# Performance work log

Hardware: AMD Instinct MI355X
Metric: run time of the kernel (lower is better)

The kernel has to match this reference:

```python
import jax, jax.numpy as jnp
import numpy as np

B, S, H, QKV, NH, MLP = 4, 2048, 512, 512, 8, 2048
HD = QKV // NH
EPS = 1e-6


def _layernorm(x):
    # LayerNorm over last dim, no affine, eps=1e-6
    mu = jnp.mean(x, axis=-1, keepdims=True)
    var = jnp.mean(jnp.square(x - mu), axis=-1, keepdims=True)
    return (x - mu) * jax.lax.rsqrt(var + EPS)


def setup_inputs() -> dict:
    key = jax.random.key(0)
    ks = jax.random.split(key, 8)
    sc_in = 1.0 / np.sqrt(H)
    sc_qkv = 1.0 / np.sqrt(QKV)
    sc_mlp = 1.0 / np.sqrt(MLP)
    return {
        "input": jax.random.normal(ks[0], (B, S, H), dtype=jnp.float32),
        "mask": jnp.ones((B, S), dtype=jnp.float32),
        "Wq": jax.random.normal(ks[1], (H, QKV), dtype=jnp.float32) * sc_in,
        "Wk": jax.random.normal(ks[2], (H, QKV), dtype=jnp.float32) * sc_in,
        "Wv": jax.random.normal(ks[3], (H, QKV), dtype=jnp.float32) * sc_in,
        "Wo": jax.random.normal(ks[4], (QKV, H), dtype=jnp.float32) * sc_qkv,
        "W1": jax.random.normal(ks[5], (H, MLP), dtype=jnp.float32) * sc_in,
        "W2": jax.random.normal(ks[6], (MLP, H), dtype=jnp.float32) * sc_mlp,
    }


def reference(input, mask, Wq, Wk, Wv, Wo, W1, W2):
    # pre-mask + pre-norm
    x = input * mask[..., None]
    x = _layernorm(x)
    # qkv projections, split heads: [B,S,QKV] -> [B,NH,S,HD]
    def heads(t):
        return t.reshape(B, S, NH, HD).transpose(0, 2, 1, 3)
    q = heads(x @ Wq) * (1.0 / np.sqrt(HD))
    k = heads(x @ Wk)
    v = heads(x @ Wv)
    logits = jnp.einsum("bhqd,bhkd->bhqk", q, k)  # [B,NH,S,S]
    amask = mask[:, None, :, None]  # 'b q -> b 1 q 1'
    logits = logits + (-100000.0) * (1.0 - amask)
    att = jax.nn.softmax(logits, axis=-1)
    out = jnp.einsum("bhqk,bhkd->bhqd", att, v)
    out = out.transpose(0, 2, 1, 3).reshape(B, S, QKV)
    x = input + out @ Wo  # residual
    x = x * mask[..., None]
    y = _layernorm(x)
    ffn = jax.nn.gelu(y @ W1, approximate=False) @ W2
    return ffn + x
```

## Files before the change

kernel.cpp:

```cpp
#include <hip/hip_runtime.h>
#include <hip/hip_bf16.h>
#include <cmath>

typedef __attribute__((ext_vector_type(8))) short bf16x8;
typedef __attribute__((ext_vector_type(4))) float f32x4;
typedef __attribute__((ext_vector_type(16))) float f32x16;
typedef unsigned short u16;
typedef unsigned int u32;

#define B_ 4
#define S_ 2048
#define H_ 512
#define NH_ 8
#define HD_ 64
#define MLP_ 2048
#define M_ (B_*S_)

__device__ __forceinline__ float bf2f(u16 u){ u32 v=((u32)u)<<16; float f; __builtin_memcpy(&f,&v,4); return f; }
__device__ __forceinline__ u16 f2bf(float f){ u32 u; __builtin_memcpy(&u,&f,4); u32 r=(u+0x7fffu+((u>>16)&1u))>>16; return (u16)r; }
__device__ __forceinline__ u32 pk2(float lo, float hi2){
  __hip_bfloat162 t = __float22bfloat162_rn(make_float2(lo, hi2));
  u32 r; __builtin_memcpy(&r, &t, 4); return r;
}

__device__ __forceinline__ float xhalf_add(float x){
  float a = x, b = x;
  asm volatile("v_permlane32_swap_b32 %0, %1" : "+v"(a), "+v"(b));
  return a + b;
}

__device__ __forceinline__ void gl16(const u16* g, u16* l) {
  __builtin_amdgcn_global_load_lds((const __attribute__((address_space(1))) u32*)(g),
                                   (__attribute__((address_space(3))) u32*)(l), 16, 0, 0);
}

__device__ __forceinline__ void gemm_core(
    const u16* __restrict__ A, const u16* __restrict__ Bt,
    int lda, int ldb, int nkt, int m0, int n0,
    u16* As, u16* Bs, f32x4 (&acc)[4][4])
{
  const int tid = threadIdx.x;
  const int lane = tid & 63;
  const int w = tid >> 6;
  const int lr = lane & 15;
  const int g  = lane >> 4;
  const int wr = w >> 1, wc = w & 1;

  const int sr = lane >> 3;
  const int scol = ((lane & 7) ^ sr) << 3;

  int aoff[2][4], boff[2][4];
#pragma unroll
  for (int m = 0; m < 4; ++m) {
    int ra = wr*64 + m*16 + lr;
    int rb = wc*64 + m*16 + lr;
#pragma unroll
    for (int kk = 0; kk < 2; ++kk) {
      aoff[kk][m] = ra*64 + (((kk*4+g) ^ (ra&7))<<3);
      boff[kk][m] = rb*64 + (((kk*4+g) ^ (rb&7))<<3);
    }
  }
  const u16* Ap = A + (size_t)m0*lda;
  const u16* Bp = Bt + (size_t)n0*ldb;

#pragma unroll
  for (int c = 0; c < 4; ++c) {
    gl16(Ap + (size_t)(w*32 + c*8 + sr)*lda + scol, As + w*2048 + c*512);
    gl16(Bp + (size_t)(w*32 + c*8 + sr)*ldb + scol, Bs + w*2048 + c*512);
  }

  for (int kt = 0; kt < nkt; ++kt) {
    const int cb = (kt & 1) * 8192;
    if (kt + 1 < nkt) {
      const int k0 = (kt + 1) << 6;
      const int nb = ((kt + 1) & 1) * 8192;
#pragma unroll
      for (int c = 0; c < 4; ++c) {
        gl16(Ap + (size_t)(w*32 + c*8 + sr)*lda + k0 + scol, As + nb + w*2048 + c*512);
        gl16(Bp + (size_t)(w*32 + c*8 + sr)*ldb + k0 + scol, Bs + nb + w*2048 + c*512);
      }
      asm volatile("s_waitcnt vmcnt(8)" ::: "memory");
    } else {
      asm volatile("s_waitcnt vmcnt(0)" ::: "memory");
    }
    __builtin_amdgcn_s_barrier();

#pragma unroll
    for (int kk = 0; kk < 2; ++kk) {
      bf16x8 af[4], bfr[4];
#pragma unroll
      for (int m = 0; m < 4; ++m) {
        af[m]  = *(const bf16x8*)(As + cb + aoff[kk][m]);
        bfr[m] = *(const bf16x8*)(Bs + cb + boff[kk][m]);
      }
#pragma unroll
      for (int m = 0; m < 4; ++m) {
#pragma unroll
        for (int n = 0; n < 4; ++n) {
          acc[m][n] = __builtin_amdgcn_mfma_f32_16x16x32_bf16(af[m], bfr[n], acc[m][n], 0, 0, 0);
        }
      }
    }
    __builtin_amdgcn_s_barrier();
  }
}

__device__ __forceinline__ void gemm_core64(
    const u16* __restrict__ A, const u16* __restrict__ Bt,
    int lda, int ldb, int nkt, int m0, int n0,
    u16* As, u16* Bs, f32x4 (&acc)[2][4])
{
  const int tid = threadIdx.x;
  const int lane = tid & 63;
  const int w = tid >> 6;
  const int lr = lane & 15;
  const int g  = lane >> 4;

  const int sr = lane >> 3;
  const int scol = ((lane & 7) ^ sr) << 3;

  int aoff[2][2], boff[2][4];
#pragma unroll
  for (int m = 0; m < 2; ++m) {
    int ra = w*32 + m*16 + lr;
#pragma unroll
    for (int kk = 0; kk < 2; ++kk) aoff[kk][m] = ra*64 + (((kk*4+g) ^ (ra&7))<<3);
  }
#pragma unroll
  for (int n = 0; n < 4; ++n) {
    int rb = n*16 + lr;
#pragma unroll
    for (int kk = 0; kk < 2; ++kk) boff[kk][n] = rb*64 + (((kk*4+g) ^ (rb&7))<<3);
  }
  const u16* Ap = A + (size_t)m0*lda;
  const u16* Bp = Bt + (size_t)n0*ldb;

#pragma unroll
  for (int c = 0; c < 4; ++c)
    gl16(Ap + (size_t)(w*32 + c*8 + sr)*lda + scol, As + w*2048 + c*512);
#pragma unroll
  for (int c = 0; c < 2; ++c)
    gl16(Bp + (size_t)(w*16 + c*8 + sr)*ldb + scol, Bs + w*1024 + c*512);

  for (int kt = 0; kt < nkt; ++kt) {
    const int cbA = (kt & 1) * 8192;
    const int cbB = (kt & 1) * 4096;
    if (kt + 1 < nkt) {
      const int k0 = (kt + 1) << 6;
      const int nbA = ((kt + 1) & 1) * 8192;
      const int nbB = ((kt + 1) & 1) * 4096;
#pragma unroll
      for (int c = 0; c < 4; ++c)
        gl16(Ap + (size_t)(w*32 + c*8 + sr)*lda + k0 + scol, As + nbA + w*2048 + c*512);
#pragma unroll
      for (int c = 0; c < 2; ++c)
        gl16(Bp + (size_t)(w*16 + c*8 + sr)*ldb + k0 + scol, Bs + nbB + w*1024 + c*512);
      asm volatile("s_waitcnt vmcnt(6)" ::: "memory");
    } else {
      asm volatile("s_waitcnt vmcnt(0)" ::: "memory");
    }
    __builtin_amdgcn_s_barrier();

#pragma unroll
    for (int kk = 0; kk < 2; ++kk) {
      bf16x8 af[2], bfr[4];
#pragma unroll
      for (int m = 0; m < 2; ++m) af[m] = *(const bf16x8*)(As + cbA + aoff[kk][m]);
#pragma unroll
      for (int n = 0; n < 4; ++n) bfr[n] = *(const bf16x8*)(Bs + cbB + boff[kk][n]);
#pragma unroll
      for (int m = 0; m < 2; ++m) {
#pragma unroll
        for (int n = 0; n < 4; ++n) {
          acc[m][n] = __builtin_amdgcn_mfma_f32_16x16x32_bf16(af[m], bfr[n], acc[m][n], 0, 0, 0);
        }
      }
    }
    __builtin_amdgcn_s_barrier();
  }
}

__global__ __launch_bounds__(256,2) void k_qkv(
    const u16* __restrict__ xn, const u16* __restrict__ wqt,
    const u16* __restrict__ wkt, const u16* __restrict__ wvt,
    u16* __restrict__ q, u16* __restrict__ k, u16* __restrict__ v)
{
  __shared__ u16 As[2*128*64], Bs[2*128*64];
  int m0 = blockIdx.x*128;
  int sel = blockIdx.y >> 2;
  int n0 = (blockIdx.y & 3)*128;
  const u16* Bt = sel==0 ? wqt : (sel==1 ? wkt : wvt);
  u16* O = sel==0 ? q : (sel==1 ? k : v);
  float alpha = (sel==0) ? 0.125f : 1.0f;
  f32x4 acc[4][4] = {};
  gemm_core(xn, Bt, H_, H_, H_/64, m0, n0, As, Bs, acc);
  const int lane = threadIdx.x&63, w = threadIdx.x>>6;
  const int lr = lane&15, g = lane>>4, wr = w>>1, wc = w&1;
#pragma unroll
  for (int m=0;m<4;++m) {
#pragma unroll
    for (int n=0;n<4;++n) {
#pragma unroll
      for (int r=0;r<4;++r) {
        int row = m0 + wr*64 + m*16 + g*4 + r;
        int col = n0 + wc*64 + n*16 + lr;
        O[(size_t)row*H_ + col] = f2bf(acc[m][n][r]*alpha);
      }
    }
  }
}

template<int EPI>
__global__ __launch_bounds__(256,2) void k_gemm(
    const u16* __restrict__ A, const u16* __restrict__ Bt, void* __restrict__ Ov,
    const float* __restrict__ aux, const float* __restrict__ maskv,
    int N, int K)
{
  __shared__ u16 As[2*128*64], Bs[2*128*64];
  int m0 = blockIdx.x*128, n0 = blockIdx.y*128;
  f32x4 acc[4][4] = {};
  gemm_core(A, Bt, K, K, K>>6, m0, n0, As, Bs, acc);
  const int lane = threadIdx.x&63, w = threadIdx.x>>6;
  const int lr = lane&15, g = lane>>4, wr = w>>1, wc = w&1;
#pragma unroll
  for (int m=0;m<4;++m) {
#pragma unroll
    for (int n=0;n<4;++n) {
#pragma unroll
      for (int r=0;r<4;++r) {
        int row = m0 + wr*64 + m*16 + g*4 + r;
        int col = n0 + wc*64 + n*16 + lr;
        float val = acc[m][n][r];
        if (EPI == 1) {
          val = 0.5f*val*(1.0f + erff(val*0.70710678118654752f));
          ((u16*)Ov)[(size_t)row*N + col] = f2bf(val);
        } else if (EPI == 2) {
          float mv = maskv[row];
          val = (aux[(size_t)row*N + col] + val)*mv;
          ((float*)Ov)[(size_t)row*N + col] = val;
        } else if (EPI == 3) {
          val += aux[(size_t)row*N + col];
          ((float*)Ov)[(size_t)row*N + col] = val;
        }
      }
    }
  }
}

template<int EPI>
__global__ __launch_bounds__(256,3) void k_gemm64(
    const u16* __restrict__ A, const u16* __restrict__ Bt, void* __restrict__ Ov,
    const float* __restrict__ aux, const float* __restrict__ maskv,
    int N, int K)
{
  __shared__ u16 As[2*128*64], Bs[2*64*64];
  int m0 = blockIdx.x*128, n0 = blockIdx.y*64;
  f32x4 acc[2][4] = {};
  gemm_core64(A, Bt, K, K, K>>6, m0, n0, As, Bs, acc);
  const int lane = threadIdx.x&63, w = threadIdx.x>>6;
  const int lr = lane&15, g = lane>>4;
#pragma unroll
  for (int m=0;m<2;++m) {
#pragma unroll
    for (int n=0;n<4;++n) {
#pragma unroll
      for (int r=0;r<4;++r) {
        int row = m0 + w*32 + m*16 + g*4 + r;
        int col = n0 + n*16 + lr;
        float val = acc[m][n][r];
        if (EPI == 2) {
          float mv = maskv[row];
          val = (aux[(size_t)row*N + col] + val)*mv;
          ((float*)Ov)[(size_t)row*N + col] = val;
        } else if (EPI == 3) {
          val += aux[(size_t)row*N + col];
          ((float*)Ov)[(size_t)row*N + col] = val;
        }
      }
    }
  }
}

template<int MASKED>
__global__ __launch_bounds__(256) void k_ln(const float* __restrict__ in,
    const float* __restrict__ mask, u16* __restrict__ out)
{
  int row = blockIdx.x*4 + (threadIdx.x>>6);
  int lane = threadIdx.x & 63;
  const f32x4* p = (const f32x4*)(in + (size_t)row*H_ + lane*8);
  f32x4 a = p[0], b = p[1];
  float mv = MASKED ? mask[row] : 1.0f;
  float x[8]; float s = 0.f, s2 = 0.f;
#pragma unroll
  for (int j=0;j<4;++j){ x[j] = a[j]*mv; x[4+j] = b[j]*mv; }
#pragma unroll
  for (int j=0;j<8;++j){ s += x[j]; s2 += x[j]*x[j]; }
#pragma unroll
  for (int m=1;m<32;m<<=1){ s += __shfl_xor(s,m); s2 += __shfl_xor(s2,m); }
  s = xhalf_add(s); s2 = xhalf_add(s2);
  float mu = s*(1.0f/H_);
  float var = s2*(1.0f/H_) - mu*mu;
  float inv = rsqrtf(var + 1e-6f);
  bf16x8 o;
#pragma unroll
  for (int j=0;j<8;++j) o[j] = (short)f2bf((x[j]-mu)*inv);
  *(bf16x8*)(out + (size_t)row*H_ + lane*8) = o;
}

__global__ void k_tr4(const float* __restrict__ s0, const float* __restrict__ s1,
                      const float* __restrict__ s2, const float* __restrict__ s3,
                      u16* __restrict__ d0, u16* __restrict__ d1,
                      u16* __restrict__ d2, u16* __restrict__ d3)
{
  __shared__ u16 t[32][33];
  const float* src = blockIdx.z==0 ? s0 : (blockIdx.z==1 ? s1 : (blockIdx.z==2 ? s2 : s3));
  u16* dst = blockIdx.z==0 ? d0 : (blockIdx.z==1 ? d1 : (blockIdx.z==2 ? d2 : d3));
  int c0 = blockIdx.x*32, r0 = blockIdx.y*32;
  int tx = threadIdx.x & 31, ty = threadIdx.x >> 5;
#pragma unroll
  for (int i=0;i<32;i+=8) t[ty+i][tx] = f2bf(src[(size_t)(r0+ty+i)*512 + c0+tx]);
  __syncthreads();
#pragma unroll
  for (int i=0;i<32;i+=8) dst[(size_t)(c0+ty+i)*512 + r0+tx] = t[tx][ty+i];
}

__global__ void k_tr(const float* __restrict__ src, u16* __restrict__ dst, int R, int C)
{
  __shared__ u16 t[32][33];
  int c0 = blockIdx.x*32, r0 = blockIdx.y*32;
  int tx = threadIdx.x & 31, ty = threadIdx.x >> 5;
#pragma unroll
  for (int i=0;i<32;i+=8) t[ty+i][tx] = f2bf(src[(size_t)(r0+ty+i)*C + c0+tx]);
  __syncthreads();
#pragma unroll
  for (int i=0;i<32;i+=8) dst[(size_t)(c0+ty+i)*R + r0+tx] = t[tx][ty+i];
}

__global__ void k_trv(const u16* __restrict__ v, u16* __restrict__ vt)
{
  __shared__ u16 t[32][33];
  int bh = blockIdx.z, b = bh>>3, h = bh&7;
  int s0 = blockIdx.x*32, d0 = blockIdx.y*32;
  int tx = threadIdx.x & 31, ty = threadIdx.x >> 5;
#pragma unroll
  for (int i=0;i<32;i+=8) t[ty+i][tx] = v[(size_t)(b*S_ + s0+ty+i)*H_ + h*HD_ + d0+tx];
  __syncthreads();
#pragma unroll
  for (int i=0;i<32;i+=8) vt[((size_t)bh*HD_ + d0+ty+i)*S_ + s0+tx] = t[tx][ty+i];
}

__global__ __launch_bounds__(256) void k_attn(
    const u16* __restrict__ q, const u16* __restrict__ kmat,
    const u16* __restrict__ vt, const float* __restrict__ mask,
    u16* __restrict__ o)
{
  __shared__ u16 Ks[2][64*64];
  __shared__ u16 Vs[2][64*64];
  __shared__ float bias[S_];
  __shared__ float lsums[4][32];

  const int tid = threadIdx.x;
  const int lane = tid & 63;
  const int w = tid >> 6;
  const int l31 = lane & 31;
  const int hi = lane >> 5;
  const int bh = blockIdx.y, b = bh >> 3, h = bh & 7;
  const int q0 = blockIdx.x * 128;

  const int sr = lane >> 3;
  const int sl = (lane & 7) ^ (sr & 7);
  const u16* ks0 = kmat + (size_t)(b*S_ + w*16 + sr)*H_ + h*HD_ + sl*8;
  const u16* ks1 = ks0 + (size_t)8*H_;
  const u16* vs0 = vt + ((size_t)bh*HD_ + w*16 + sr)*S_ + sl*8;
  const u16* vs1 = vs0 + (size_t)8*S_;

  {
    u16* kd = &Ks[0][0] + w*1024;
    u16* vd = &Vs[0][0] + w*1024;
    gl16(ks0, kd); gl16(ks1, kd + 512);
    gl16(vs0, vd); gl16(vs1, vd + 512);
  }

  for (int j = tid; j < S_; j += 256) bias[j] = -100000.0f * (1.0f - mask[b*S_ + j]);

  bf16x8 qf[4];
  {
    const u16* qp = q + (size_t)(b*S_ + q0 + w*32 + l31)*H_ + h*HD_ + hi*8;
#pragma unroll
    for (int ds = 0; ds < 4; ++ds) qf[ds] = *(const bf16x8*)(qp + ds*16);
  }

  f32x16 po0 = {}, po1 = {};
  float mreg = -1e30f, lsum = 0.f;

  __syncthreads();

  for (int jt = 0; jt < 32; ++jt) {
    const int buf = jt & 1;
    if (jt < 31) {
      const int j0 = (jt + 1) * 64;
      u16* kd = &Ks[buf ^ 1][0] + w*1024;
      u16* vd = &Vs[buf ^ 1][0] + w*1024;
      gl16(ks0 + (size_t)j0*H_, kd); gl16(ks1 + (size_t)j0*H_, kd + 512);
      gl16(vs0 + j0, vd);            gl16(vs1 + j0, vd + 512);
      asm volatile("s_waitcnt vmcnt(4)" ::: "memory");
    } else {
      asm volatile("s_waitcnt vmcnt(0)" ::: "memory");
    }
    __builtin_amdgcn_s_barrier();

    const u16* kt  = &Ks[buf][0];
    const u16* vtl = &Vs[buf][0];

    f32x16 s0, s1;
    const float* bp = &bias[jt*64 + hi*4];
#pragma unroll
    for (int kb = 0; kb < 2; ++kb) {
      f32x16 acc;
#pragma unroll
      for (int g2 = 0; g2 < 4; ++g2) {
        f32x4 b4 = *(const f32x4*)(bp + kb*32 + g2*8);
        acc[g2*4+0] = b4[0]; acc[g2*4+1] = b4[1];
        acc[g2*4+2] = b4[2]; acc[g2*4+3] = b4[3];
      }
      const int key = kb*32 + l31;
      const u16* kr = kt + key*64;
      __builtin_amdgcn_s_setprio(1);
#pragma unroll
      for (int ds = 0; ds < 4; ++ds) {
        bf16x8 kf = *(const bf16x8*)(kr + (((ds*2 + hi) ^ (key & 7)) << 3));
        acc = __builtin_amdgcn_mfma_f32_32x32x16_bf16(kf, qf[ds], acc, 0, 0, 0);
      }
      __builtin_amdgcn_s_setprio(0);
      if (kb == 0) s0 = acc; else s1 = acc;
    }

    float mx = s0[0];
#pragma unroll
    for (int r = 1; r < 16; ++r) mx = fmaxf(mx, s0[r]);
#pragma unroll
    for (int r = 0; r < 16; ++r) mx = fmaxf(mx, s1[r]);
    mx = fmaxf(mx, __shfl_xor(mx, 32));
    if (__any(mx > mreg + 8.0f)) {
      float mn = fmaxf(mreg, mx);
      float sc = __expf(mreg - mn);
      lsum *= sc;
#pragma unroll
      for (int r = 0; r < 16; ++r) { po0[r] *= sc; po1[r] *= sc; }
      mreg = mn;
    }
    float ps = 0.f;
#pragma unroll
    for (int r = 0; r < 16; ++r) { float p = __expf(s0[r]-mreg); s0[r] = p; ps += p; }
#pragma unroll
    for (int r = 0; r < 16; ++r) { float p = __expf(s1[r]-mreg); s1[r] = p; ps += p; }
    ps += __shfl_xor(ps, 32);
    lsum += ps;

#pragma unroll
    for (int kb = 0; kb < 2; ++kb) {
      const f32x16& sv = kb ? s1 : s0;
      u32 w01 = pk2(sv[0],  sv[1]);
      u32 w23 = pk2(sv[2],  sv[3]);
      u32 w45 = pk2(sv[4],  sv[5]);
      u32 w67 = pk2(sv[6],  sv[7]);
      asm volatile("v_permlane32_swap_b32 %0, %1" : "+v"(w01), "+v"(w45));
      asm volatile("v_permlane32_swap_b32 %0, %1" : "+v"(w23), "+v"(w67));
      u32 w89 = pk2(sv[8],  sv[9]);
      u32 wab = pk2(sv[10], sv[11]);
      u32 wcd = pk2(sv[12], sv[13]);
      u32 wef = pk2(sv[14], sv[15]);
      asm volatile("v_permlane32_swap_b32 %0, %1" : "+v"(w89), "+v"(wcd));
      asm volatile("v_permlane32_swap_b32 %0, %1" : "+v"(wab), "+v"(wef));
      union { u32 wrd[4]; bf16x8 v; } f0, f1;
      f0.wrd[0]=w01; f0.wrd[1]=w23; f0.wrd[2]=w45; f0.wrd[3]=w67;
      f1.wrd[0]=w89; f1.wrd[1]=wab; f1.wrd[2]=wcd; f1.wrd[3]=wef;
      __builtin_amdgcn_s_setprio(1);
#pragma unroll
      for (int ks = 0; ks < 2; ++ks) {
        bf16x8 pa = ks ? f1.v : f0.v;
#pragma unroll
        for (int nb = 0; nb < 2; ++nb) {
          int dd = nb*32 + l31;
          int slot = ((kb*4 + ks*2 + hi) ^ (dd & 7)) << 3;
          bf16x8 vf = *(const bf16x8*)(vtl + dd*64 + slot);
          if (nb == 0) po0 = __builtin_amdgcn_mfma_f32_32x32x16_bf16(pa, vf, po0, 0,0,0);
          else         po1 = __builtin_amdgcn_mfma_f32_32x32x16_bf16(pa, vf, po1, 0,0,0);
        }
      }
      __builtin_amdgcn_s_setprio(0);
    }
    __builtin_amdgcn_s_barrier();
  }

  if (hi == 0) lsums[w][l31] = lsum;
  f32x4 li[4];
#pragma unroll
  for (int g2i = 0; g2i < 4; ++g2i) {
    f32x4 t = *(const f32x4*)&lsums[w][g2i*8 + hi*4];
    li[g2i][0] = 1.0f/t[0]; li[g2i][1] = 1.0f/t[1];
    li[g2i][2] = 1.0f/t[2]; li[g2i][3] = 1.0f/t[3];
  }
  u16* op = o + (size_t)(b*S_ + q0 + w*32)*H_ + h*HD_;
#pragma unroll
  for (int nb = 0; nb < 2; ++nb) {
#pragma unroll
    for (int r = 0; r < 16; ++r) {
      int row = (r&3) + 8*(r>>2) + 4*hi;
      float val = (nb ? po1[r] : po0[r]) * li[r>>2][r&3];
      op[(size_t)row*H_ + nb*32 + l31] = f2bf(val);
    }
  }
}

extern "C" void kernel_launch(void* const* d_in, const int* in_sizes, int n_in,
                              void* d_out, int out_size, void* d_ws, size_t ws_size,
                              hipStream_t stream) {
  const float* input = (const float*)d_in[0];
  const float* mask  = (const float*)d_in[1];
  const float* Wq = (const float*)d_in[2];
  const float* Wk = (const float*)d_in[3];
  const float* Wv = (const float*)d_in[4];
  const float* Wo = (const float*)d_in[5];
  const float* W1 = (const float*)d_in[6];
  const float* W2 = (const float*)d_in[7];
  float* out = (float*)d_out;
  u16* ws = (u16*)d_ws;

  u16* wqt = ws;
  u16* wkt = wqt + 262144;
  u16* wvt = wkt + 262144;
  u16* wot = wvt + 262144;
  u16* w1t = wot + 262144;
  u16* w2t = w1t + 1048576;
  u16* xn  = w2t + 1048576;
  u16* q   = xn  + 4194304;
  u16* k   = q   + 4194304;
  u16* v   = k   + 4194304;
  u16* vt  = v   + 4194304;
  u16*   attn = xn;
  float* x2f  = (float*)q;
  u16*   y    = v;
  u16*   h1   = vt;

  dim3 blk(256);
  k_tr4<<<dim3(16,16,4), blk, 0, stream>>>(Wq, Wk, Wv, Wo, wqt, wkt, wvt, wot);
  k_tr<<<dim3(64,16), blk, 0, stream>>>(W1, w1t, 512, 2048);
  k_tr<<<dim3(16,64), blk, 0, stream>>>(W2, w2t, 2048, 512);

  k_ln<1><<<2048, blk, 0, stream>>>(input, mask, xn);
  k_qkv<<<dim3(64,12), blk, 0, stream>>>(xn, wqt, wkt, wvt, q, k, v);
  k_trv<<<dim3(64,2,32), blk, 0, stream>>>(v, vt);
  k_attn<<<dim3(16,32), blk, 0, stream>>>(q, k, vt, mask, attn);
  k_gemm64<2><<<dim3(64,8), blk, 0, stream>>>(attn, wot, (void*)x2f, input, mask, 512, 512);
  k_ln<0><<<2048, blk, 0, stream>>>(x2f, nullptr, y);
  k_gemm<1><<<dim3(64,16), blk, 0, stream>>>(y, w1t, (void*)h1, nullptr, nullptr, 2048, 512);
  k_gemm64<3><<<dim3(64,8), blk, 0, stream>>>(h1, w2t, (void*)out, x2f, nullptr, 512, 2048);
}
```

Baseline: 192.7 us.

## Split attention keys into two halves with a combine pass, precompute mask bias

Attention now splits the key range into two halves over a new grid dimension, doubling block count from 512 to 1024 to fill more CUs. Each half writes unnormalized bf16 partial outputs plus per-row max and sum, and a new combine kernel merges them with log-sum-exp weights. The mask bias is precomputed once per batch into global memory with a flag, so bias loads are skipped when the mask has no zeros. This adds extra global traffic for the partials, an extra bf16 rounding, and two more kernel launches.

New measurement: 200.8 us. 1.04x slower.

```diff
diff --git a/kernel.cpp b/kernel.cpp
--- a/kernel.cpp
+++ b/kernel.cpp
@@ -349,15 +349,33 @@
   for (int i=0;i<32;i+=8) vt[((size_t)bh*HD_ + d0+ty+i)*S_ + s0+tx] = t[tx][ty+i];
 }
 
+__global__ void k_prep(const float* __restrict__ mask, float* __restrict__ biasf,
+                       u32* __restrict__ hb)
+{
+  __shared__ u32 f;
+  int b = blockIdx.x;
+  if (threadIdx.x == 0) f = 0;
+  __syncthreads();
+  bool any = false;
+  for (int j = threadIdx.x; j < S_; j += 256) {
+    float bv = -100000.0f * (1.0f - mask[b*S_ + j]);
+    biasf[b*S_ + j] = bv;
+    any |= (bv != 0.0f);
+  }
+  if (__ballot(any) != 0ull && (threadIdx.x & 63) == 0) atomicOr(&f, 1u);
+  __syncthreads();
+  if (threadIdx.x == 0) hb[b] = f;
+}
+
 __global__ __launch_bounds__(256) void k_attn(
     const u16* __restrict__ q, const u16* __restrict__ kmat,
-    const u16* __restrict__ vt, const float* __restrict__ mask,
-    u16* __restrict__ o)
+    const u16* __restrict__ vt, const float* __restrict__ biasf,
+    const u32* __restrict__ hb,
+    u16* __restrict__ pO0, u16* __restrict__ pO1,
+    float2* __restrict__ ml0, float2* __restrict__ ml1)
 {
   __shared__ u16 Ks[2][64*64];
   __shared__ u16 Vs[2][64*64];
-  __shared__ float bias[S_];
-  __shared__ float lsums[4][32];
 
   const int tid = threadIdx.x;
   const int lane = tid & 63;
@@ -366,12 +384,14 @@
   const int hi = lane >> 5;
   const int bh = blockIdx.y, b = bh >> 3, h = bh & 7;
   const int q0 = blockIdx.x * 128;
+  const int half = blockIdx.z;
+  const int k0g = half * 1024;
 
   const int sr = lane >> 3;
   const int sl = (lane & 7) ^ (sr & 7);
-  const u16* ks0 = kmat + (size_t)(b*S_ + w*16 + sr)*H_ + h*HD_ + sl*8;
+  const u16* ks0 = kmat + (size_t)(b*S_ + k0g + w*16 + sr)*H_ + h*HD_ + sl*8;
   const u16* ks1 = ks0 + (size_t)8*H_;
-  const u16* vs0 = vt + ((size_t)bh*HD_ + w*16 + sr)*S_ + sl*8;
+  const u16* vs0 = vt + ((size_t)bh*HD_ + w*16 + sr)*S_ + k0g + sl*8;
   const u16* vs1 = vs0 + (size_t)8*S_;
 
   {
@@ -381,7 +401,7 @@
     gl16(vs0, vd); gl16(vs1, vd + 512);
   }
 
-  for (int j = tid; j < S_; j += 256) bias[j] = -100000.0f * (1.0f - mask[b*S_ + j]);
+  const u32 hasb = hb[b];
 
   bf16x8 qf[4];
   {
@@ -395,9 +415,9 @@
 
   __syncthreads();
 
-  for (int jt = 0; jt < 32; ++jt) {
+  for (int jt = 0; jt < 16; ++jt) {
     const int buf = jt & 1;
-    if (jt < 31) {
+    if (jt < 15) {
       const int j0 = (jt + 1) * 64;
       u16* kd = &Ks[buf ^ 1][0] + w*1024;
       u16* vd = &Vs[buf ^ 1][0] + w*1024;
@@ -413,15 +433,17 @@
     const u16* vtl = &Vs[buf][0];
 
     f32x16 s0, s1;
-    const float* bp = &bias[jt*64 + hi*4];
 #pragma unroll
     for (int kb = 0; kb < 2; ++kb) {
-      f32x16 acc;
-#pragma unroll
-      for (int g2 = 0; g2 < 4; ++g2) {
-        f32x4 b4 = *(const f32x4*)(bp + kb*32 + g2*8);
-        acc[g2*4+0] = b4[0]; acc[g2*4+1] = b4[1];
-        acc[g2*4+2] = b4[2]; acc[g2*4+3] = b4[3];
+      f32x16 acc = {};
+      if (hasb) {
+        const float* bp = biasf + b*S_ + k0g + jt*64 + kb*32 + hi*4;
+#pragma unroll
+        for (int g2 = 0; g2 < 4; ++g2) {
+          f32x4 b4 = *(const f32x4*)(bp + g2*8);
+          acc[g2*4+0] = b4[0]; acc[g2*4+1] = b4[1];
+          acc[g2*4+2] = b4[2]; acc[g2*4+3] = b4[3];
+        }
       }
       const int key = kb*32 + l31;
       const u16* kr = kt + key*64;
@@ -493,24 +515,41 @@
     __builtin_amdgcn_s_barrier();
   }
 
-  if (hi == 0) lsums[w][l31] = lsum;
-  f32x4 li[4];
-#pragma unroll
-  for (int g2i = 0; g2i < 4; ++g2i) {
-    f32x4 t = *(const f32x4*)&lsums[w][g2i*8 + hi*4];
-    li[g2i][0] = 1.0f/t[0]; li[g2i][1] = 1.0f/t[1];
-    li[g2i][2] = 1.0f/t[2]; li[g2i][3] = 1.0f/t[3];
-  }
-  u16* op = o + (size_t)(b*S_ + q0 + w*32)*H_ + h*HD_;
+  u16* pOp = half ? pO1 : pO0;
+  float2* mlp = half ? ml1 : ml0;
+  u16* op = pOp + ((size_t)bh*S_ + q0 + w*32)*HD_;
 #pragma unroll
   for (int nb = 0; nb < 2; ++nb) {
 #pragma unroll
     for (int r = 0; r < 16; ++r) {
       int row = (r&3) + 8*(r>>2) + 4*hi;
-      float val = (nb ? po1[r] : po0[r]) * li[r>>2][r&3];
-      op[(size_t)row*H_ + nb*32 + l31] = f2bf(val);
-    }
-  }
+      op[(size_t)row*HD_ + nb*32 + l31] = f2bf(nb ? po1[r] : po0[r]);
+    }
+  }
+  if (hi == 0) mlp[(size_t)bh*S_ + q0 + w*32 + l31] = make_float2(mreg, lsum);
+}
+
+__global__ __launch_bounds__(256) void k_combine(
+    const u16* __restrict__ pO0, const u16* __restrict__ pO1,
+    const float2* __restrict__ ml0, const float2* __restrict__ ml1,
+    u16* __restrict__ o)
+{
+  const int bh = blockIdx.y, b = bh >> 3, h = bh & 7;
+  const int s = blockIdx.x*32 + (threadIdx.x >> 3);
+  const int dg = (threadIdx.x & 7) * 8;
+  float2 a = ml0[(size_t)bh*S_ + s];
+  float2 c = ml1[(size_t)bh*S_ + s];
+  float M = fmaxf(a.x, c.x);
+  float w0 = __expf(a.x - M), w1 = __expf(c.x - M);
+  float inv = 1.0f / (a.y*w0 + c.y*w1);
+  w0 *= inv; w1 *= inv;
+  bf16x8 f0 = *(const bf16x8*)(pO0 + ((size_t)bh*S_ + s)*HD_ + dg);
+  bf16x8 f1 = *(const bf16x8*)(pO1 + ((size_t)bh*S_ + s)*HD_ + dg);
+  bf16x8 r;
+#pragma unroll
+  for (int j = 0; j < 8; ++j)
+    r[j] = (short)f2bf(bf2f((u16)f0[j])*w0 + bf2f((u16)f1[j])*w1);
+  *(bf16x8*)(o + ((size_t)(b*S_ + s))*H_ + h*HD_ + dg) = r;
 }
 
 extern "C" void kernel_launch(void* const* d_in, const int* in_sizes, int n_in,
@@ -538,6 +577,12 @@
   u16* k   = q   + 4194304;
   u16* v   = k   + 4194304;
   u16* vt  = v   + 4194304;
+  u16*    pO0  = v;
+  u16*    pO1  = vt + 4194304;
+  float2* ml0  = (float2*)(pO1 + 4194304);
+  float2* ml1  = ml0 + 65536;
+  float*  biasf = (float*)(ml1 + 65536);
+  u32*    hbp   = (u32*)(biasf + B_*S_);
   u16*   attn = xn;
   float* x2f  = (float*)q;
   u16*   y    = v;
@@ -547,11 +592,13 @@
   k_tr4<<<dim3(16,16,4), blk, 0, stream>>>(Wq, Wk, Wv, Wo, wqt, wkt, wvt, wot);
   k_tr<<<dim3(64,16), blk, 0, stream>>>(W1, w1t, 512, 2048);
   k_tr<<<dim3(16,64), blk, 0, stream>>>(W2, w2t, 2048, 512);
+  k_prep<<<dim3(B_), blk, 0, stream>>>(mask, biasf, hbp);
 
   k_ln<1><<<2048, blk, 0, stream>>>(input, mask, xn);
   k_qkv<<<dim3(64,12), blk, 0, stream>>>(xn, wqt, wkt, wvt, q, k, v);
   k_trv<<<dim3(64,2,32), blk, 0, stream>>>(v, vt);
-  k_attn<<<dim3(16,32), blk, 0, stream>>>(q, k, vt, mask, attn);
+  k_attn<<<dim3(16,32,2), blk, 0, stream>>>(q, k, vt, biasf, hbp, pO0, pO1, ml0, ml1);
+  k_combine<<<dim3(64,32), blk, 0, stream>>>(pO0, pO1, ml0, ml1, attn);
   k_gemm64<2><<<dim3(64,8), blk, 0, stream>>>(attn, wot, (void*)x2f, input, mask, 512, 512);
   k_ln<0><<<2048, blk, 0, stream>>>(x2f, nullptr, y);
   k_gemm<1><<<dim3(64,16), blk, 0, stream>>>(y, w1t, (void*)h1, nullptr, nullptr, 2048, 512);
```

## Fuse V transpose into QKV epilogue, use exp2 softmax, merge weight transposes

Applied to the files above, without the earlier changes.

The QKV GEMM epilogue now writes V directly in transposed per-head layout, which removes the separate k_trv kernel and its extra read and write of V. Q is pre-scaled by log2(e) and the mask bias is scaled to match, so the attention softmax can use the native exp2 instruction instead of __expf. The two MLP weight-transpose launches are merged into a single launch. In exchange, the transposed V stores are 8-byte writes strided by S, which may coalesce poorly.

After: 184.2 us. -4.4%, faster.

```diff
diff --git a/kernel.cpp b/kernel.cpp
--- a/kernel.cpp
+++ b/kernel.cpp
@@ -3,6 +3,7 @@
 #include <cmath>
 
 typedef __attribute__((ext_vector_type(8))) short bf16x8;
+typedef __attribute__((ext_vector_type(4))) short u16x4;
 typedef __attribute__((ext_vector_type(4))) float f32x4;
 typedef __attribute__((ext_vector_type(16))) float f32x16;
 typedef unsigned short u16;
@@ -15,6 +16,7 @@
 #define HD_ 64
 #define MLP_ 2048
 #define M_ (B_*S_)
+#define LOG2E 1.44269504088896340736f
 
 __device__ __forceinline__ float bf2f(u16 u){ u32 v=((u32)u)<<16; float f; __builtin_memcpy(&f,&v,4); return f; }
 __device__ __forceinline__ u16 f2bf(float f){ u32 u; __builtin_memcpy(&u,&f,4); u32 r=(u+0x7fffu+((u>>16)&1u))>>16; return (u16)r; }
@@ -183,28 +185,45 @@
 __global__ __launch_bounds__(256,2) void k_qkv(
     const u16* __restrict__ xn, const u16* __restrict__ wqt,
     const u16* __restrict__ wkt, const u16* __restrict__ wvt,
-    u16* __restrict__ q, u16* __restrict__ k, u16* __restrict__ v)
+    u16* __restrict__ q, u16* __restrict__ k, u16* __restrict__ vt)
 {
   __shared__ u16 As[2*128*64], Bs[2*128*64];
   int m0 = blockIdx.x*128;
   int sel = blockIdx.y >> 2;
   int n0 = (blockIdx.y & 3)*128;
   const u16* Bt = sel==0 ? wqt : (sel==1 ? wkt : wvt);
-  u16* O = sel==0 ? q : (sel==1 ? k : v);
-  float alpha = (sel==0) ? 0.125f : 1.0f;
+  float alpha = (sel==0) ? 0.125f*LOG2E : 1.0f;
   f32x4 acc[4][4] = {};
   gemm_core(xn, Bt, H_, H_, H_/64, m0, n0, As, Bs, acc);
   const int lane = threadIdx.x&63, w = threadIdx.x>>6;
   const int lr = lane&15, g = lane>>4, wr = w>>1, wc = w&1;
-#pragma unroll
-  for (int m=0;m<4;++m) {
-#pragma unroll
-    for (int n=0;n<4;++n) {
-#pragma unroll
-      for (int r=0;r<4;++r) {
-        int row = m0 + wr*64 + m*16 + g*4 + r;
-        int col = n0 + wc*64 + n*16 + lr;
-        O[(size_t)row*H_ + col] = f2bf(acc[m][n][r]*alpha);
+  if (sel == 2) {
+#pragma unroll
+    for (int m=0;m<4;++m) {
+#pragma unroll
+      for (int n=0;n<4;++n) {
+        int rowb = m0 + wr*64 + m*16 + g*4;
+        int col  = n0 + wc*64 + n*16 + lr;
+        int b = rowb >> 11, s = rowb & 2047;
+        int h = col >> 6, d = col & 63;
+        u16x4 t;
+#pragma unroll
+        for (int r=0;r<4;++r) t[r] = (short)f2bf(acc[m][n][r]);
+        *(u16x4*)(vt + ((size_t)((b*NH_ + h)*HD_ + d))*S_ + s) = t;
+      }
+    }
+  } else {
+    u16* O = sel==0 ? q : k;
+#pragma unroll
+    for (int m=0;m<4;++m) {
+#pragma unroll
+      for (int n=0;n<4;++n) {
+#pragma unroll
+        for (int r=0;r<4;++r) {
+          int row = m0 + wr*64 + m*16 + g*4 + r;
+          int col = n0 + wc*64 + n*16 + lr;
+          O[(size_t)row*H_ + col] = f2bf(acc[m][n][r]*alpha);
+        }
       }
     }
   }
@@ -324,29 +343,23 @@
   for (int i=0;i<32;i+=8) dst[(size_t)(c0+ty+i)*512 + r0+tx] = t[tx][ty+i];
 }
 
-__global__ void k_tr(const float* __restrict__ src, u16* __restrict__ dst, int R, int C)
+__global__ void k_tr2(const float* __restrict__ W1, const float* __restrict__ W2,
+                      u16* __restrict__ d1, u16* __restrict__ d2)
 {
   __shared__ u16 t[32][33];
-  int c0 = blockIdx.x*32, r0 = blockIdx.y*32;
+  int z = blockIdx.z;
+  const float* src = z ? W2 : W1;
+  u16* dst = z ? d2 : d1;
+  int R = z ? 2048 : 512;
+  int C = z ? 512 : 2048;
+  int c0 = (z ? blockIdx.y : blockIdx.x) * 32;
+  int r0 = (z ? blockIdx.x : blockIdx.y) * 32;
   int tx = threadIdx.x & 31, ty = threadIdx.x >> 5;
 #pragma unroll
   for (int i=0;i<32;i+=8) t[ty+i][tx] = f2bf(src[(size_t)(r0+ty+i)*C + c0+tx]);
   __syncthreads();
 #pragma unroll
   for (int i=0;i<32;i+=8) dst[(size_t)(c0+ty+i)*R + r0+tx] = t[tx][ty+i];
-}
-
-__global__ void k_trv(const u16* __restrict__ v, u16* __restrict__ vt)
-{
-  __shared__ u16 t[32][33];
-  int bh = blockIdx.z, b = bh>>3, h = bh&7;
-  int s0 = blockIdx.x*32, d0 = blockIdx.y*32;
-  int tx = threadIdx.x & 31, ty = threadIdx.x >> 5;
-#pragma unroll
-  for (int i=0;i<32;i+=8) t[ty+i][tx] = v[(size_t)(b*S_ + s0+ty+i)*H_ + h*HD_ + d0+tx];
-  __syncthreads();
-#pragma unroll
-  for (int i=0;i<32;i+=8) vt[((size_t)bh*HD_ + d0+ty+i)*S_ + s0+tx] = t[tx][ty+i];
 }
 
 __global__ __launch_bounds__(256) void k_attn(
@@ -381,7 +394,7 @@
     gl16(vs0, vd); gl16(vs1, vd + 512);
   }
 
-  for (int j = tid; j < S_; j += 256) bias[j] = -100000.0f * (1.0f - mask[b*S_ + j]);
+  for (int j = tid; j < S_; j += 256) bias[j] = -144269.5f * (1.0f - mask[b*S_ + j]);
 
   bf16x8 qf[4];
   {
@@ -443,7 +456,7 @@
     mx = fmaxf(mx, __shfl_xor(mx, 32));
     if (__any(mx > mreg + 8.0f)) {
       float mn = fmaxf(mreg, mx);
-      float sc = __expf(mreg - mn);
+      float sc = __builtin_amdgcn_exp2f(mreg - mn);
       lsum *= sc;
 #pragma unroll
       for (int r = 0; r < 16; ++r) { po0[r] *= sc; po1[r] *= sc; }
@@ -451,9 +464,9 @@
     }
     float ps = 0.f;
 #pragma unroll
-    for (int r = 0; r < 16; ++r) { float p = __expf(s0[r]-mreg); s0[r] = p; ps += p; }
-#pragma unroll
-    for (int r = 0; r < 16; ++r) { float p = __expf(s1[r]-mreg); s1[r] = p; ps += p; }
+    for (int r = 0; r < 16; ++r) { float p = __builtin_amdgcn_exp2f(s0[r]-mreg); s0[r] = p; ps += p; }
+#pragma unroll
+    for (int r = 0; r < 16; ++r) { float p = __builtin_amdgcn_exp2f(s1[r]-mreg); s1[r] = p; ps += p; }
     ps += __shfl_xor(ps, 32);
     lsum += ps;
 
@@ -545,12 +558,10 @@
 
   dim3 blk(256);
   k_tr4<<<dim3(16,16,4), blk, 0, stream>>>(Wq, Wk, Wv, Wo, wqt, wkt, wvt, wot);
-  k_tr<<<dim3(64,16), blk, 0, stream>>>(W1, w1t, 512, 2048);
-  k_tr<<<dim3(16,64), blk, 0, stream>>>(W2, w2t, 2048, 512);
+  k_tr2<<<dim3(64,16,2), blk, 0, stream>>>(W1, W2, w1t, w2t);
 
   k_ln<1><<<2048, blk, 0, stream>>>(input, mask, xn);
-  k_qkv<<<dim3(64,12), blk, 0, stream>>>(xn, wqt, wkt, wvt, q, k, v);
-  k_trv<<<dim3(64,2,32), blk, 0, stream>>>(v, vt);
+  k_qkv<<<dim3(64,12), blk, 0, stream>>>(xn, wqt, wkt, wvt, q, k, vt);
   k_attn<<<dim3(16,32), blk, 0, stream>>>(q, k, vt, mask, attn);
   k_gemm64<2><<<dim3(64,8), blk, 0, stream>>>(attn, wot, (void*)x2f, input, mask, 512, 512);
   k_ln<0><<<2048, blk, 0, stream>>>(x2f, nullptr, y);
```
